# Optimization experiments

Measured on AMD Instinct MI355X. Metric: run time of the kernel, lower is better.

## Reference

```python
import jax, jax.numpy as jnp
import numpy as np

B, S, D, H, L, MLP, WIN = 4, 1024, 256, 8, 2, 1024, 64
HD = D // H
NEG = -1e9  # emulates -inf additive mask; exp underflows to exact 0

_idx = jnp.arange(S)
BAND = jnp.where(jnp.abs(_idx[:, None] - _idx[None, :]) <= WIN, 0.0, NEG).astype(jnp.float32)


def setup_inputs() -> dict:
    key = jax.random.key(0)
    ks = iter(jax.random.split(key, 16))
    r = lambda shape, s=0.02: jax.random.normal(next(ks), shape, dtype=jnp.float32) * s
    return {
        "x": jax.random.normal(next(ks), (B, S, D), dtype=jnp.float32),
        "scale": jnp.ones((1,), jnp.float32) * (D ** -0.5),
        "Win_a": r((L, 3 * D, D)), "bin_a": jnp.zeros((L, 3 * D), jnp.float32),
        "Wout_a": r((L, D, D)), "bout_a": jnp.zeros((L, D), jnp.float32),
        "Win_e": r((L, 3 * D, D)), "bin_e": jnp.zeros((L, 3 * D), jnp.float32),
        "Wout_e": r((L, D, D)), "bout_e": jnp.zeros((L, D), jnp.float32),
        "ln1_g": jnp.ones((L, D), jnp.float32), "ln1_b": jnp.zeros((L, D), jnp.float32),
        "ln2_g": jnp.ones((L, D), jnp.float32), "ln2_b": jnp.zeros((L, D), jnp.float32),
        "W1": r((L, MLP, D)), "b1": jnp.zeros((L, MLP), jnp.float32),
        "W2": r((L, D, MLP)), "b2": jnp.zeros((L, D), jnp.float32),
        "lnf_g": jnp.ones((D,), jnp.float32), "lnf_b": jnp.zeros((D,), jnp.float32),
    }


def _layernorm(x, g, b, eps=1e-5):
    m = jnp.mean(x, axis=-1, keepdims=True)
    v = jnp.mean(jnp.square(x - m), axis=-1, keepdims=True)
    return (x - m) * jax.lax.rsqrt(v + eps) * g + b


def _mha(x, Win, bin_, Wout, bout, mask=None):
    # torch nn.MultiheadAttention (batch_first=True), dropout=0
    b, s, _ = x.shape
    qkv = x @ Win.T + bin_                       # (b, s, 3D)
    q, k, v = jnp.split(qkv, 3, axis=-1)
    split = lambda t: t.reshape(b, s, H, HD).transpose(0, 2, 1, 3)  # (b, H, s, HD)
    q, k, v = split(q), split(k), split(v)
    scores = jnp.einsum('bhqd,bhkd->bhqk', q, k) / np.float32(np.sqrt(HD))
    if mask is not None:
        scores = scores + mask
    attn = jax.nn.softmax(scores, axis=-1)
    out = jnp.einsum('bhqk,bhkd->bhqd', attn, v).transpose(0, 2, 1, 3).reshape(b, s, D)
    return out @ Wout.T + bout


def reference(x, scale, Win_a, bin_a, Wout_a, bout_a, Win_e, bin_e, Wout_e, bout_e,
              ln1_g, ln1_b, ln2_g, ln2_b, W1, b1, W2, b2, lnf_g, lnf_b):
    # ScaledSinusoidalPositionalEncoding returns arange(S)*scale, shape (S,1)
    pos = jnp.arange(S, dtype=jnp.float32) * scale[0]   # (S,)
    x = x + pos[:, None]                                 # broadcast (B,S,D)+(S,1)
    for l in range(L):
        xi = _mha(x, Win_a[l], bin_a[l], Wout_a[l], bout_a[l])
        x = _layernorm(x + xi, ln1_g[l], ln1_b[l])
        xe = _mha(x, Win_e[l], bin_e[l], Wout_e[l], bout_e[l], mask=BAND)
        attended = _layernorm(x + xe, ln2_g[l], ln2_b[l])
        h = jax.nn.gelu(attended @ W1[l].T + b1[l], approximate=False)
        x = attended + h @ W2[l].T + b2[l]
    return _layernorm(x, lnf_g, lnf_b)
```

## Files before the change

kernel.cpp:

```cpp
#include <hip/hip_runtime.h>
#include <math.h>

#define BB 4
#define SS 1024
#define DD 256
#define HH 8
#define HD 32
#define D3 768
#define MLP 1024
#define NTOK (BB * SS)
#define NSEG 4

typedef __attribute__((ext_vector_type(8))) short short8;
typedef __attribute__((ext_vector_type(4))) float f32x4;

__device__ __forceinline__ unsigned short f2bfu(float f) {
    union { float f; unsigned i; } u; u.f = f;
    unsigned r = u.i + 0x7fffu + ((u.i >> 16) & 1u);
    return (unsigned short)(r >> 16);
}
__device__ __forceinline__ float bfu2f(unsigned short h) {
    union { unsigned i; float f; } u; u.i = ((unsigned)h) << 16; return u.f;
}

#define W_TOT 2097152
#define WL0   196608
__global__ __launch_bounds__(256) void conv_weights(
    const float* __restrict__ a0, const float* __restrict__ a1,
    const float* __restrict__ a2, const float* __restrict__ a3,
    const float* __restrict__ a4, const float* __restrict__ a5,
    unsigned short* __restrict__ out, unsigned short* __restrict__ out_lo)
{
    int i = blockIdx.x * 256 + threadIdx.x;
    const float* s; int off;
    if      (i <  393216) { s = a0; off = 0;       }
    else if (i <  524288) { s = a1; off = 393216;  }
    else if (i <  917504) { s = a2; off = 524288;  }
    else if (i < 1048576) { s = a3; off = 917504;  }
    else if (i < 1572864) { s = a4; off = 1048576; }
    else                  { s = a5; off = 1572864; }
    float v = s[i - off];
    unsigned short h = f2bfu(v);
    out[i] = h;
    if (i < WL0) out_lo[i] = f2bfu(v - bfu2f(h));
}

__global__ __launch_bounds__(256) void add_pos_kernel(
    const float* __restrict__ x, const float* __restrict__ scale,
    float* __restrict__ out, unsigned short* __restrict__ outh,
    unsigned short* __restrict__ outl, int n)
{
    int i = blockIdx.x * 256 + threadIdx.x;
    if (i >= n) return;
    int s = (i >> 8) & (SS - 1);
    float v = x[i] + (float)s * scale[0];
    out[i] = v;
    unsigned short h = f2bfu(v);
    outh[i] = h;
    outl[i] = f2bfu(v - bfu2f(h));
}

__device__ __forceinline__ size_t vt_index(int row, int col512) {
    int b = row >> 10, s = row & (SS - 1);
    int h = col512 >> 5, d = col512 & (HD - 1);
    return (((size_t)b * HH + h) * HD + d) * SS + s;
}

#define LDP 40
__global__ __launch_bounds__(256) void gemm_mfma(
    const unsigned short* __restrict__ A, const unsigned short* __restrict__ W,
    const float* __restrict__ bias, const float* __restrict__ resid,
    float* __restrict__ outf, unsigned short* __restrict__ outb,
    unsigned short* __restrict__ vth,
    int M, int N, int K, int act)
{
    __shared__ __align__(16) unsigned short As[64 * LDP];
    __shared__ __align__(16) unsigned short Bs[128 * LDP];
    const int t = threadIdx.x;
    const int lane = t & 63, wave = t >> 6;
    const int wr = wave >> 1, wc = wave & 1;
    const int m0 = blockIdx.y * 64, n0 = blockIdx.x * 128;
    const int sr = t >> 2;
    const int sc = (t & 3) * 8;

    const unsigned short* Ag = A + (size_t)(m0 + sr) * K + sc;
    const unsigned short* Wg = W + (size_t)(n0 + sr) * K + sc;

    f32x4 acc[2][4];
    #pragma unroll
    for (int i = 0; i < 2; i++)
        #pragma unroll
        for (int j = 0; j < 4; j++)
            acc[i][j] = (f32x4){0.f, 0.f, 0.f, 0.f};

    const int lm = lane & 15, lk = (lane >> 4) * 8;

    uint4 a0 = *(const uint4*)(Ag);
    uint4 b0 = *(const uint4*)(Wg);
    uint4 b1 = *(const uint4*)(Wg + (size_t)64 * K);

    for (int k0 = 0; k0 < K; k0 += 32) {
        __syncthreads();
        *(uint4*)&As[sr * LDP + sc]        = a0;
        *(uint4*)&Bs[sr * LDP + sc]        = b0;
        *(uint4*)&Bs[(sr + 64) * LDP + sc] = b1;
        __syncthreads();
        if (k0 + 32 < K) {
            a0 = *(const uint4*)(Ag + k0 + 32);
            b0 = *(const uint4*)(Wg + k0 + 32);
            b1 = *(const uint4*)(Wg + (size_t)64 * K + k0 + 32);
        }

        short8 af[2], bf[4];
        #pragma unroll
        for (int i = 0; i < 2; i++)
            af[i] = *(const short8*)&As[(wr * 32 + i * 16 + lm) * LDP + lk];
        #pragma unroll
        for (int j = 0; j < 4; j++)
            bf[j] = *(const short8*)&Bs[(wc * 64 + j * 16 + lm) * LDP + lk];
        #pragma unroll
        for (int i = 0; i < 2; i++)
            #pragma unroll
            for (int j = 0; j < 4; j++)
                acc[i][j] = __builtin_amdgcn_mfma_f32_16x16x32_bf16(
                    af[i], bf[j], acc[i][j], 0, 0, 0);
    }

    const int lq = lane >> 4;
    #pragma unroll
    for (int j = 0; j < 4; j++) {
        int col = n0 + wc * 64 + j * 16 + lm;
        float bv = bias[col];
        #pragma unroll
        for (int i = 0; i < 2; i++) {
            #pragma unroll
            for (int r = 0; r < 4; r++) {
                int row = m0 + wr * 32 + i * 16 + lq * 4 + r;
                float v = acc[i][j][r] + bv;
                if (act) v = 0.5f * v * (1.0f + erff(v * 0.70710678118654752f));
                if (vth && col >= 2 * DD) {
                    vth[vt_index(row, col - 2 * DD)] = f2bfu(v);
                } else {
                    size_t idx = (size_t)row * N + col;
                    if (resid) v += resid[idx];
                    if (outf) outf[idx] = v;
                    if (outb) outb[idx] = f2bfu(v);
                }
            }
        }
    }
}

__global__ __launch_bounds__(256) void gemm_wout_combine(
    const float* __restrict__ Of, const float2* __restrict__ Ml,
    const unsigned short* __restrict__ W, const float* __restrict__ bias,
    float* __restrict__ outf)
{
    __shared__ __align__(16) unsigned short As[64 * LDP];
    __shared__ __align__(16) unsigned short Bs[128 * LDP];
    const int t = threadIdx.x;
    const int lane = t & 63, wave = t >> 6;
    const int wr = wave >> 1, wc = wave & 1;
    const int m0 = blockIdx.y * 64, n0 = blockIdx.x * 128;
    const int sr = t >> 2;
    const int sc = (t & 3) * 8;
    const int token = m0 + sr;

    const unsigned short* Wg = W + (size_t)(n0 + sr) * DD + sc;

    f32x4 acc[2][4];
    #pragma unroll
    for (int i = 0; i < 2; i++)
        #pragma unroll
        for (int j = 0; j < 4; j++)
            acc[i][j] = (f32x4){0.f, 0.f, 0.f, 0.f};

    const int lm = lane & 15, lk = (lane >> 4) * 8;

    for (int k0 = 0; k0 < DD; k0 += 32) {
        const int h = (k0 + sc) >> 5;
        float2 ml[NSEG];
        float M = -1e30f;
        #pragma unroll
        for (int s = 0; s < NSEG; s++) {
            ml[s] = Ml[((size_t)s * NTOK + token) * HH + h];
            M = fmaxf(M, ml[s].x);
        }
        float wgt[NSEG]; float denom = 0.f;
        #pragma unroll
        for (int s = 0; s < NSEG; s++) {
            wgt[s] = __expf(ml[s].x - M);
            denom += ml[s].y * wgt[s];
        }
        const float inv = 1.0f / denom;
        float a8[8] = {};
        #pragma unroll
        for (int s = 0; s < NSEG; s++) {
            const float* p = Of + ((size_t)s * NTOK + token) * DD + k0 + sc;
            float4 x0 = *(const float4*)p;
            float4 x1 = *(const float4*)(p + 4);
            a8[0] += x0.x * wgt[s]; a8[1] += x0.y * wgt[s];
            a8[2] += x0.z * wgt[s]; a8[3] += x0.w * wgt[s];
            a8[4] += x1.x * wgt[s]; a8[5] += x1.y * wgt[s];
            a8[6] += x1.z * wgt[s]; a8[7] += x1.w * wgt[s];
        }
        unsigned short ab[8];
        #pragma unroll
        for (int c = 0; c < 8; c++) ab[c] = f2bfu(a8[c] * inv);

        uint4 b0 = *(const uint4*)(Wg + k0);
        uint4 b1 = *(const uint4*)(Wg + (size_t)64 * DD + k0);
        __syncthreads();
        #pragma unroll
        for (int c = 0; c < 8; c++) As[sr * LDP + sc + c] = ab[c];
        *(uint4*)&Bs[sr * LDP + sc]        = b0;
        *(uint4*)&Bs[(sr + 64) * LDP + sc] = b1;
        __syncthreads();

        short8 af[2], bf[4];
        #pragma unroll
        for (int i = 0; i < 2; i++)
            af[i] = *(const short8*)&As[(wr * 32 + i * 16 + lm) * LDP + lk];
        #pragma unroll
        for (int j = 0; j < 4; j++)
            bf[j] = *(const short8*)&Bs[(wc * 64 + j * 16 + lm) * LDP + lk];
        #pragma unroll
        for (int i = 0; i < 2; i++)
            #pragma unroll
            for (int j = 0; j < 4; j++)
                acc[i][j] = __builtin_amdgcn_mfma_f32_16x16x32_bf16(
                    af[i], bf[j], acc[i][j], 0, 0, 0);
    }

    const int lq = lane >> 4;
    #pragma unroll
    for (int j = 0; j < 4; j++) {
        int col = n0 + wc * 64 + j * 16 + lm;
        float bv = bias[col];
        #pragma unroll
        for (int i = 0; i < 2; i++) {
            #pragma unroll
            for (int r = 0; r < 4; r++) {
                int row = m0 + wr * 32 + i * 16 + lq * 4 + r;
                outf[(size_t)row * DD + col] = acc[i][j][r] + bv;
            }
        }
    }
}

__global__ __launch_bounds__(256) void gemm_mfma_split(
    const unsigned short* __restrict__ Ah, const unsigned short* __restrict__ Al,
    const unsigned short* __restrict__ Wh, const unsigned short* __restrict__ Wl,
    const float* __restrict__ bias,
    unsigned short* __restrict__ outh, unsigned short* __restrict__ outl,
    unsigned short* __restrict__ vth, unsigned short* __restrict__ vtl,
    int M, int N, int K)
{
    __shared__ __align__(16) unsigned short Ash[64 * LDP];
    __shared__ __align__(16) unsigned short Asl[64 * LDP];
    __shared__ __align__(16) unsigned short Bsh[128 * LDP];
    __shared__ __align__(16) unsigned short Bsl[128 * LDP];
    const int t = threadIdx.x;
    const int lane = t & 63, wave = t >> 6;
    const int wr = wave >> 1, wc = wave & 1;
    const int m0 = blockIdx.y * 64, n0 = blockIdx.x * 128;
    const int sr = t >> 2;
    const int sc = (t & 3) * 8;

    const size_t oA = (size_t)(m0 + sr) * K + sc;
    const size_t oW = (size_t)(n0 + sr) * K + sc;

    f32x4 acc[2][4];
    #pragma unroll
    for (int i = 0; i < 2; i++)
        #pragma unroll
        for (int j = 0; j < 4; j++)
            acc[i][j] = (f32x4){0.f, 0.f, 0.f, 0.f};

    const int lm = lane & 15, lk = (lane >> 4) * 8;

    uint4 ah0 = *(const uint4*)(Ah + oA);
    uint4 al0 = *(const uint4*)(Al + oA);
    uint4 bh0 = *(const uint4*)(Wh + oW);
    uint4 bh1 = *(const uint4*)(Wh + oW + (size_t)64 * K);
    uint4 bl0 = *(const uint4*)(Wl + oW);
    uint4 bl1 = *(const uint4*)(Wl + oW + (size_t)64 * K);

    for (int k0 = 0; k0 < K; k0 += 32) {
        __syncthreads();
        *(uint4*)&Ash[sr * LDP + sc]        = ah0;
        *(uint4*)&Asl[sr * LDP + sc]        = al0;
        *(uint4*)&Bsh[sr * LDP + sc]        = bh0;
        *(uint4*)&Bsh[(sr + 64) * LDP + sc] = bh1;
        *(uint4*)&Bsl[sr * LDP + sc]        = bl0;
        *(uint4*)&Bsl[(sr + 64) * LDP + sc] = bl1;
        __syncthreads();
        if (k0 + 32 < K) {
            ah0 = *(const uint4*)(Ah + oA + k0 + 32);
            al0 = *(const uint4*)(Al + oA + k0 + 32);
            bh0 = *(const uint4*)(Wh + oW + k0 + 32);
            bh1 = *(const uint4*)(Wh + oW + (size_t)64 * K + k0 + 32);
            bl0 = *(const uint4*)(Wl + oW + k0 + 32);
            bl1 = *(const uint4*)(Wl + oW + (size_t)64 * K + k0 + 32);
        }

        short8 afh[2], afl[2], bfh[4], bfl[4];
        #pragma unroll
        for (int i = 0; i < 2; i++) {
            afh[i] = *(const short8*)&Ash[(wr * 32 + i * 16 + lm) * LDP + lk];
            afl[i] = *(const short8*)&Asl[(wr * 32 + i * 16 + lm) * LDP + lk];
        }
        #pragma unroll
        for (int j = 0; j < 4; j++) {
            bfh[j] = *(const short8*)&Bsh[(wc * 64 + j * 16 + lm) * LDP + lk];
            bfl[j] = *(const short8*)&Bsl[(wc * 64 + j * 16 + lm) * LDP + lk];
        }
        #pragma unroll
        for (int i = 0; i < 2; i++)
            #pragma unroll
            for (int j = 0; j < 4; j++) {
                acc[i][j] = __builtin_amdgcn_mfma_f32_16x16x32_bf16(
                    afl[i], bfh[j], acc[i][j], 0, 0, 0);
                acc[i][j] = __builtin_amdgcn_mfma_f32_16x16x32_bf16(
                    afh[i], bfl[j], acc[i][j], 0, 0, 0);
                acc[i][j] = __builtin_amdgcn_mfma_f32_16x16x32_bf16(
                    afh[i], bfh[j], acc[i][j], 0, 0, 0);
            }
    }

    const int lq = lane >> 4;
    #pragma unroll
    for (int j = 0; j < 4; j++) {
        int col = n0 + wc * 64 + j * 16 + lm;
        float bv = bias[col];
        #pragma unroll
        for (int i = 0; i < 2; i++) {
            #pragma unroll
            for (int r = 0; r < 4; r++) {
                int row = m0 + wr * 32 + i * 16 + lq * 4 + r;
                float v = acc[i][j][r] + bv;
                unsigned short h = f2bfu(v);
                unsigned short lo = f2bfu(v - bfu2f(h));
                if (col >= 2 * DD) {
                    size_t vi = vt_index(row, col - 2 * DD);
                    vth[vi] = h; vtl[vi] = lo;
                } else {
                    size_t idx = (size_t)row * N + col;
                    outh[idx] = h; outl[idx] = lo;
                }
            }
        }
    }
}

__global__ __launch_bounds__(256) void attn_split(
    const unsigned short* __restrict__ qkvh,
    const unsigned short* __restrict__ qkvl,
    const unsigned short* __restrict__ vth,
    const unsigned short* __restrict__ vtl,
    float* __restrict__ Of, float2* __restrict__ Ml)
{
    __shared__ __align__(16) unsigned short Ks [64 * 40];
    __shared__ __align__(16) unsigned short Vt [32 * 72];
    __shared__ __align__(16) unsigned short Ps [64 * 72];
    __shared__ __align__(16) unsigned short Ksl[64 * 40];
    __shared__ __align__(16) unsigned short Vtl[32 * 72];

    const int t = threadIdx.x;
    const int wave = t >> 6, lane = t & 63;
    const int lm = lane & 15, quad = lane >> 4;
    const int i0 = blockIdx.x * 64, h = blockIdx.y;
    const int z = blockIdx.z;
    const int b = z >> 2, seg = z & (NSEG - 1);
    const int sr = t >> 2, sc8 = (t & 3) * 8;
    const int vd = t >> 3, vs8 = (t & 7) * 8;

    const size_t qoff = ((size_t)(b * SS) + i0 + 16 * wave + lm) * D3 + h * HD + quad * 8;
    short8 qh = *(const short8*)(qkvh + qoff);
    short8 ql = *(const short8*)(qkvl + qoff);

    const unsigned short* Kg  = qkvh + (size_t)(b * SS) * D3 + DD + h * HD;
    const unsigned short* Klg = qkvl + (size_t)(b * SS) * D3 + DD + h * HD;
    const unsigned short* Vg  = vth + ((size_t)b * HH + h) * HD * SS;
    const unsigned short* Vlg = vtl + ((size_t)b * HH + h) * HD * SS;

    float m[4], l[4];
    f32x4 o[2];
    #pragma unroll
    for (int r = 0; r < 4; r++) { m[r] = -1e30f; l[r] = 0.f; }
    o[0] = (f32x4){0.f, 0.f, 0.f, 0.f};
    o[1] = (f32x4){0.f, 0.f, 0.f, 0.f};

    const int per = (SS / 64) / NSEG;
    const int s0 = seg * per, s1 = s0 + per - 1;
    const float scl = 0.17677669529663688f;

    short8 kreg  = *(const short8*)(Kg  + (size_t)(s0 * 64 + sr) * D3 + sc8);
    short8 kregl = *(const short8*)(Klg + (size_t)(s0 * 64 + sr) * D3 + sc8);
    short8 vreg  = *(const short8*)(Vg  + (size_t)vd * SS + s0 * 64 + vs8);
    short8 vregl = *(const short8*)(Vlg + (size_t)vd * SS + s0 * 64 + vs8);

    for (int kt = s0; kt <= s1; kt++) {
        const int k0 = kt * 64;
        __syncthreads();
        *(short8*)&Ks [sr * 40 + sc8] = kreg;
        *(short8*)&Ksl[sr * 40 + sc8] = kregl;
        *(short8*)&Vt [vd * 72 + vs8] = vreg;
        *(short8*)&Vtl[vd * 72 + vs8] = vregl;
        __syncthreads();
        if (kt < s1) {
            kreg  = *(const short8*)(Kg  + (size_t)(k0 + 64 + sr) * D3 + sc8);
            kregl = *(const short8*)(Klg + (size_t)(k0 + 64 + sr) * D3 + sc8);
            vreg  = *(const short8*)(Vg  + (size_t)vd * SS + k0 + 64 + vs8);
            vregl = *(const short8*)(Vlg + (size_t)vd * SS + k0 + 64 + vs8);
        }

        f32x4 s[4];
        #pragma unroll
        for (int cb = 0; cb < 4; cb++) {
            short8 kf  = *(const short8*)&Ks [(16 * cb + lm) * 40 + quad * 8];
            short8 kfl = *(const short8*)&Ksl[(16 * cb + lm) * 40 + quad * 8];
            f32x4 a = (f32x4){0.f, 0.f, 0.f, 0.f};
            a = __builtin_amdgcn_mfma_f32_16x16x32_bf16(ql, kf,  a, 0, 0, 0);
            a = __builtin_amdgcn_mfma_f32_16x16x32_bf16(qh, kfl, a, 0, 0, 0);
            a = __builtin_amdgcn_mfma_f32_16x16x32_bf16(qh, kf,  a, 0, 0, 0);
            s[cb] = a;
        }

        #pragma unroll
        for (int r = 0; r < 4; r++) {
            float s0r = s[0][r] * scl, s1r = s[1][r] * scl;
            float s2r = s[2][r] * scl, s3r = s[3][r] * scl;
            float tm = fmaxf(fmaxf(s0r, s1r), fmaxf(s2r, s3r));
            tm = fmaxf(tm, __shfl_xor(tm, 1, 64));
            tm = fmaxf(tm, __shfl_xor(tm, 2, 64));
            tm = fmaxf(tm, __shfl_xor(tm, 4, 64));
            tm = fmaxf(tm, __shfl_xor(tm, 8, 64));
            float mn = fmaxf(m[r], tm);
            float alpha = __expf(m[r] - mn);
            float p0 = __expf(s0r - mn), p1 = __expf(s1r - mn);
            float p2 = __expf(s2r - mn), p3 = __expf(s3r - mn);
            float ps = p0 + p1 + p2 + p3;
            ps += __shfl_xor(ps, 1, 64);
            ps += __shfl_xor(ps, 2, 64);
            ps += __shfl_xor(ps, 4, 64);
            ps += __shfl_xor(ps, 8, 64);
            l[r] = l[r] * alpha + ps;
            o[0][r] *= alpha;
            o[1][r] *= alpha;
            m[r] = mn;
            const int pr = (16 * wave + quad * 4 + r) * 72 + lm;
            Ps[pr +  0] = f2bfu(p0);
            Ps[pr + 16] = f2bfu(p1);
            Ps[pr + 32] = f2bfu(p2);
            Ps[pr + 48] = f2bfu(p3);
        }

        #pragma unroll
        for (int kc = 0; kc < 2; kc++) {
            short8 pf = *(const short8*)&Ps[(16 * wave + lm) * 72 + 32 * kc + quad * 8];
            #pragma unroll
            for (int nh = 0; nh < 2; nh++) {
                short8 vf  = *(const short8*)&Vt [(16 * nh + lm) * 72 + 32 * kc + quad * 8];
                short8 vfl = *(const short8*)&Vtl[(16 * nh + lm) * 72 + 32 * kc + quad * 8];
                o[nh] = __builtin_amdgcn_mfma_f32_16x16x32_bf16(pf, vf,  o[nh], 0, 0, 0);
                o[nh] = __builtin_amdgcn_mfma_f32_16x16x32_bf16(pf, vfl, o[nh], 0, 0, 0);
            }
        }
    }

    #pragma unroll
    for (int r = 0; r < 4; r++) {
        int row = i0 + 16 * wave + quad * 4 + r;
        size_t base = ((size_t)seg * NTOK + b * SS + row) * DD + h * HD + lm;
        Of[base]      = o[0][r];
        Of[base + 16] = o[1][r];
        if (lm == 0)
            Ml[((size_t)seg * NTOK + b * SS + row) * HH + h] =
                make_float2(m[r], l[r]);
    }
}

__global__ __launch_bounds__(256) void attn_fixed(
    const unsigned short* __restrict__ qkvh,
    const unsigned short* __restrict__ vth,
    unsigned short* __restrict__ outb,
    float* __restrict__ Of, float2* __restrict__ Ml,
    int win, int nseg)
{
    __shared__ __align__(16) unsigned short Ks[64 * 40];
    __shared__ __align__(16) unsigned short Vt[32 * 72];
    __shared__ __align__(16) unsigned short Ps[64 * 72];

    const int t = threadIdx.x;
    const int wave = t >> 6, lane = t & 63;
    const int lm = lane & 15, quad = lane >> 4;
    const int i0 = blockIdx.x * 64, h = blockIdx.y;
    const int z = blockIdx.z;
    const int b = z / nseg, seg = z - b * nseg;
    const int sr = t >> 2, sc8 = (t & 3) * 8;
    const int vd = t >> 3, vs8 = (t & 7) * 8;

    const size_t qoff = ((size_t)(b * SS) + i0 + 16 * wave + lm) * D3 + h * HD + quad * 8;
    short8 qh = *(const short8*)(qkvh + qoff);

    const unsigned short* Kg = qkvh + (size_t)(b * SS) * D3 + DD + h * HD;
    const unsigned short* Vg = vth + ((size_t)b * HH + h) * HD * SS;

    float l[4] = {0.f, 0.f, 0.f, 0.f};
    f32x4 o[2];
    o[0] = (f32x4){0.f, 0.f, 0.f, 0.f};
    o[1] = (f32x4){0.f, 0.f, 0.f, 0.f};

    int t0 = 0, t1 = SS / 64 - 1;
    const bool masked = (win < SS);
    if (masked) {
        t0 = (i0 - win) >> 6;        if (t0 < 0) t0 = 0;
        t1 = (i0 + 63 + win) >> 6;   if (t1 > SS / 64 - 1) t1 = SS / 64 - 1;
    }
    const int per = (t1 - t0 + nseg) / nseg;
    const int s0 = t0 + seg * per;
    const int s1 = (s0 + per - 1 < t1) ? (s0 + per - 1) : t1;
    const float scl = 0.17677669529663688f;
    const float M0 = 32.0f;

    short8 kreg = *(const short8*)(Kg + (size_t)(s0 * 64 + sr) * D3 + sc8);
    short8 vreg = *(const short8*)(Vg + (size_t)vd * SS + s0 * 64 + vs8);

    for (int kt = s0; kt <= s1; kt++) {
        const int k0 = kt * 64;
        __syncthreads();
        *(short8*)&Ks[sr * 40 + sc8] = kreg;
        *(short8*)&Vt[vd * 72 + vs8] = vreg;
        __syncthreads();
        if (kt < s1) {
            kreg = *(const short8*)(Kg + (size_t)(k0 + 64 + sr) * D3 + sc8);
            vreg = *(const short8*)(Vg + (size_t)vd * SS + k0 + 64 + vs8);
        }

        f32x4 s[4];
        #pragma unroll
        for (int cb = 0; cb < 4; cb++) {
            short8 kf = *(const short8*)&Ks[(16 * cb + lm) * 40 + quad * 8];
            f32x4 a = (f32x4){0.f, 0.f, 0.f, 0.f};
            a = __builtin_amdgcn_mfma_f32_16x16x32_bf16(qh, kf, a, 0, 0, 0);
            s[cb] = a;
        }

        #pragma unroll
        for (int r = 0; r < 4; r++) {
            float p[4];
            #pragma unroll
            for (int cb = 0; cb < 4; cb++) {
                float v = s[cb][r] * scl;
                if (masked) {
                    int di = (i0 + 16 * wave + quad * 4 + r) - (k0 + 16 * cb + lm);
                    if (di > win || di < -win) v = -1e30f;
                }
                p[cb] = __expf(v - M0);
            }
            l[r] += p[0] + p[1] + p[2] + p[3];
            const int pr = (16 * wave + quad * 4 + r) * 72 + lm;
            Ps[pr +  0] = f2bfu(p[0]);
            Ps[pr + 16] = f2bfu(p[1]);
            Ps[pr + 32] = f2bfu(p[2]);
            Ps[pr + 48] = f2bfu(p[3]);
        }

        #pragma unroll
        for (int kc = 0; kc < 2; kc++) {
            short8 pf = *(const short8*)&Ps[(16 * wave + lm) * 72 + 32 * kc + quad * 8];
            #pragma unroll
            for (int nh = 0; nh < 2; nh++) {
                short8 vf = *(const short8*)&Vt[(16 * nh + lm) * 72 + 32 * kc + quad * 8];
                o[nh] = __builtin_amdgcn_mfma_f32_16x16x32_bf16(pf, vf, o[nh], 0, 0, 0);
            }
        }
    }

    #pragma unroll
    for (int r = 0; r < 4; r++) {
        l[r] += __shfl_xor(l[r], 1, 64);
        l[r] += __shfl_xor(l[r], 2, 64);
        l[r] += __shfl_xor(l[r], 4, 64);
        l[r] += __shfl_xor(l[r], 8, 64);
    }

    if (nseg == 1) {
        #pragma unroll
        for (int r = 0; r < 4; r++) {
            float invl = 1.0f / l[r];
            size_t base = ((size_t)(b * SS) + i0 + 16 * wave + quad * 4 + r) * DD + h * HD + lm;
            outb[base]      = f2bfu(o[0][r] * invl);
            outb[base + 16] = f2bfu(o[1][r] * invl);
        }
    } else {
        #pragma unroll
        for (int r = 0; r < 4; r++) {
            int row = i0 + 16 * wave + quad * 4 + r;
            size_t base = ((size_t)seg * NTOK + b * SS + row) * DD + h * HD + lm;
            Of[base]      = o[0][r];
            Of[base + 16] = o[1][r];
            if (lm == 0)
                Ml[((size_t)seg * NTOK + b * SS + row) * HH + h] =
                    make_float2(M0, l[r]);
        }
    }
}

__global__ __launch_bounds__(256) void ln_kernel(
    const float* __restrict__ a, const float* __restrict__ r,
    const float* __restrict__ g, const float* __restrict__ bt,
    float* __restrict__ outf, unsigned short* __restrict__ outb)
{
    const int wave = threadIdx.x >> 6, lane = threadIdx.x & 63;
    const int row = blockIdx.x * 4 + wave;
    const size_t base = (size_t)row * DD + lane * 4;
    float4 v = *(const float4*)(a + base);
    if (r) {
        float4 rv = *(const float4*)(r + base);
        v.x += rv.x; v.y += rv.y; v.z += rv.z; v.w += rv.w;
    }
    float s = v.x + v.y + v.z + v.w;
    #pragma unroll
    for (int off = 1; off < 64; off <<= 1) s += __shfl_xor(s, off, 64);
    float mean = s * (1.0f / 256.0f);
    float4 dv = { v.x - mean, v.y - mean, v.z - mean, v.w - mean };
    float s2 = dv.x * dv.x + dv.y * dv.y + dv.z * dv.z + dv.w * dv.w;
    #pragma unroll
    for (int off = 1; off < 64; off <<= 1) s2 += __shfl_xor(s2, off, 64);
    float rst = rsqrtf(s2 * (1.0f / 256.0f) + 1e-5f);
    float4 g4 = *(const float4*)(g + lane * 4);
    float4 b4 = *(const float4*)(bt + lane * 4);
    float4 ov = { dv.x * rst * g4.x + b4.x, dv.y * rst * g4.y + b4.y,
                  dv.z * rst * g4.z + b4.z, dv.w * rst * g4.w + b4.w };
    if (outf) *(float4*)(outf + base) = ov;
    if (outb) {
        ushort4 u = { f2bfu(ov.x), f2bfu(ov.y), f2bfu(ov.z), f2bfu(ov.w) };
        *(ushort4*)(outb + base) = u;
    }
}

extern "C" void kernel_launch(void* const* d_in, const int* in_sizes, int n_in,
                              void* d_out, int out_size, void* d_ws, size_t ws_size,
                              hipStream_t stream)
{
    const float* xin   = (const float*)d_in[0];
    const float* scale = (const float*)d_in[1];
    const float* Win_a = (const float*)d_in[2];
    const float* bin_a = (const float*)d_in[3];
    const float* Wout_a= (const float*)d_in[4];
    const float* bout_a= (const float*)d_in[5];
    const float* Win_e = (const float*)d_in[6];
    const float* bin_e = (const float*)d_in[7];
    const float* Wout_e= (const float*)d_in[8];
    const float* bout_e= (const float*)d_in[9];
    const float* ln1_g = (const float*)d_in[10];
    const float* ln1_b = (const float*)d_in[11];
    const float* ln2_g = (const float*)d_in[12];
    const float* ln2_b = (const float*)d_in[13];
    const float* W1    = (const float*)d_in[14];
    const float* b1    = (const float*)d_in[15];
    const float* W2    = (const float*)d_in[16];
    const float* b2    = (const float*)d_in[17];
    const float* lnf_g = (const float*)d_in[18];
    const float* lnf_b = (const float*)d_in[19];

    char* ws = (char*)d_ws;
    float* X    = (float*)ws;                     ws += (size_t)NTOK * DD * 4;
    float* X2   = (float*)ws;                     ws += (size_t)NTOK * DD * 4;
    float* P    = (float*)ws;                     ws += (size_t)NTOK * DD * 4;
    unsigned short* Xb   = (unsigned short*)ws;   ws += (size_t)NTOK * DD * 2;
    unsigned short* Xlb  = (unsigned short*)ws;   ws += (size_t)NTOK * DD * 2;
    unsigned short* X2b  = (unsigned short*)ws;   ws += (size_t)NTOK * DD * 2;
    unsigned short* ATb  = (unsigned short*)ws;   ws += (size_t)NTOK * DD * 2;
    unsigned short* QKVb = (unsigned short*)ws;   ws += (size_t)NTOK * D3 * 2;
    unsigned short* QKVl = (unsigned short*)ws;   ws += (size_t)NTOK * D3 * 2;
    unsigned short* VTh  = (unsigned short*)ws;   ws += (size_t)NTOK * DD * 2;
    unsigned short* VTl  = (unsigned short*)ws;   ws += (size_t)NTOK * DD * 2;
    unsigned short* HMLb = (unsigned short*)ws;   ws += (size_t)NTOK * MLP * 2;
    unsigned short* Wb   = (unsigned short*)ws;   ws += (size_t)W_TOT * 2;
    unsigned short* Wl0  = (unsigned short*)ws;   ws += (size_t)WL0 * 2;
    float2* Ml           = (float2*)ws;           ws += (size_t)NSEG * NTOK * HH * 8;
    float* Of            = (float*)ws;            ws += (size_t)NSEG * NTOK * DD * 4;

    unsigned short* WinA_b  = Wb + 0;
    unsigned short* WoutA_b = Wb + 393216;
    unsigned short* WinE_b  = Wb + 524288;
    unsigned short* WoutE_b = Wb + 917504;
    unsigned short* W1_b    = Wb + 1048576;
    unsigned short* W2_b    = Wb + 1572864;

    conv_weights<<<W_TOT / 256, 256, 0, stream>>>(
        Win_a, Wout_a, Win_e, Wout_e, W1, W2, Wb, Wl0);
    add_pos_kernel<<<(NTOK * DD + 255) / 256, 256, 0, stream>>>(
        xin, scale, X, Xb, Xlb, NTOK * DD);

    float* cur = X;            float* oth = X2;
    unsigned short* curb = Xb; unsigned short* othb = X2b;

    for (int l = 0; l < 2; l++) {
        if (l == 0) {
            gemm_mfma_split<<<dim3(D3 / 128, NTOK / 64), 256, 0, stream>>>(
                Xb, Xlb, WinA_b, Wl0, bin_a, QKVb, QKVl, VTh, VTl, NTOK, D3, DD);
            attn_split<<<dim3(SS / 64, HH, BB * NSEG), 256, 0, stream>>>(
                QKVb, QKVl, VTh, VTl, Of, Ml);
        } else {
            gemm_mfma<<<dim3(D3 / 128, NTOK / 64), 256, 0, stream>>>(
                curb, WinA_b + (size_t)l * D3 * DD, bin_a + (size_t)l * D3,
                nullptr, nullptr, QKVb, VTh, NTOK, D3, DD, 0);
            attn_fixed<<<dim3(SS / 64, HH, BB * NSEG), 256, 0, stream>>>(
                QKVb, VTh, nullptr, Of, Ml, 1 << 28, NSEG);
        }
        gemm_wout_combine<<<dim3(DD / 128, NTOK / 64), 256, 0, stream>>>(
            Of, Ml, WoutA_b + (size_t)l * DD * DD, bout_a + (size_t)l * DD, P);
        ln_kernel<<<NTOK / 4, 256, 0, stream>>>(
            P, cur, ln1_g + l * DD, ln1_b + l * DD, oth, othb);

        gemm_mfma<<<dim3(D3 / 128, NTOK / 64), 256, 0, stream>>>(
            othb, WinE_b + (size_t)l * D3 * DD, bin_e + (size_t)l * D3,
            nullptr, nullptr, QKVb, VTh, NTOK, D3, DD, 0);
        attn_fixed<<<dim3(SS / 64, HH, BB), 256, 0, stream>>>(
            QKVb, VTh, ATb, nullptr, nullptr, 64, 1);
        gemm_mfma<<<dim3(DD / 128, NTOK / 64), 256, 0, stream>>>(
            ATb, WoutE_b + (size_t)l * DD * DD, bout_e + (size_t)l * DD,
            nullptr, P, nullptr, nullptr, NTOK, DD, DD, 0);
        ln_kernel<<<NTOK / 4, 256, 0, stream>>>(
            P, oth, ln2_g + l * DD, ln2_b + l * DD, cur, curb);

        gemm_mfma<<<dim3(MLP / 128, NTOK / 64), 256, 0, stream>>>(
            curb, W1_b + (size_t)l * MLP * DD, b1 + (size_t)l * MLP,
            nullptr, nullptr, HMLb, nullptr, NTOK, MLP, DD, 1);
        gemm_mfma<<<dim3(DD / 128, NTOK / 64), 256, 0, stream>>>(
            HMLb, W2_b + (size_t)l * DD * MLP, b2 + (size_t)l * DD,
            cur, oth, othb, nullptr, NTOK, DD, MLP, 0);

        float* tf = cur; cur = oth; oth = tf;
        unsigned short* tb = curb; curb = othb; othb = tb;
    }

    ln_kernel<<<NTOK / 4, 256, 0, stream>>>(cur, nullptr, lnf_g, lnf_b,
                                            (float*)d_out, nullptr);
}
```

Before: 351.5 us.

## Fuse LayerNorm into full-row output GEMMs and drop low-precision V split

Adds a templated gemm_ln kernel in which each block computes a full 256-wide output row tile, so it can add bias and residual and apply LayerNorm in the epilogue. This replaces the separate Wout GEMM (or Wout-combine) plus ln_kernel pairs, and also fuses the final W2 GEMM with the final LayerNorm. The fp32 intermediate P round trip and several launches go away. It also removes the bf16 low-part correction for V in the layer-0 split-precision attention, halving its V loads and PV MFMAs at some accuracy cost. The trade-off is that the fused GEMMs launch only 64 blocks, each with more accumulators, which reduces parallelism.

```diff
diff --git a/kernel.cpp b/kernel.cpp
--- a/kernel.cpp
+++ b/kernel.cpp
@@ -151,100 +151,171 @@
     }
 }
 
-__global__ __launch_bounds__(256) void gemm_wout_combine(
+template<bool COMBINE>
+__global__ __launch_bounds__(256) void gemm_ln(
+    const unsigned short* __restrict__ A,
     const float* __restrict__ Of, const float2* __restrict__ Ml,
     const unsigned short* __restrict__ W, const float* __restrict__ bias,
-    float* __restrict__ outf)
+    const float* __restrict__ resid,
+    const float* __restrict__ g, const float* __restrict__ bt,
+    float* __restrict__ outf, unsigned short* __restrict__ outb, int K)
 {
     __shared__ __align__(16) unsigned short As[64 * LDP];
-    __shared__ __align__(16) unsigned short Bs[128 * LDP];
+    __shared__ __align__(16) unsigned short Bs[256 * LDP];
+    __shared__ float rsum[2][64];
+    __shared__ float rsum2[2][64];
     const int t = threadIdx.x;
     const int lane = t & 63, wave = t >> 6;
     const int wr = wave >> 1, wc = wave & 1;
-    const int m0 = blockIdx.y * 64, n0 = blockIdx.x * 128;
+    const int m0 = blockIdx.x * 64;
     const int sr = t >> 2;
     const int sc = (t & 3) * 8;
     const int token = m0 + sr;
 
-    const unsigned short* Wg = W + (size_t)(n0 + sr) * DD + sc;
-
-    f32x4 acc[2][4];
+    const unsigned short* Ag = COMBINE ? nullptr : A + (size_t)(m0 + sr) * K + sc;
+    const unsigned short* Wg = W + (size_t)sr * K + sc;
+
+    f32x4 acc[2][8];
     #pragma unroll
     for (int i = 0; i < 2; i++)
         #pragma unroll
-        for (int j = 0; j < 4; j++)
+        for (int j = 0; j < 8; j++)
             acc[i][j] = (f32x4){0.f, 0.f, 0.f, 0.f};
 
     const int lm = lane & 15, lk = (lane >> 4) * 8;
 
-    for (int k0 = 0; k0 < DD; k0 += 32) {
-        const int h = (k0 + sc) >> 5;
-        float2 ml[NSEG];
-        float M = -1e30f;
-        #pragma unroll
-        for (int s = 0; s < NSEG; s++) {
-            ml[s] = Ml[((size_t)s * NTOK + token) * HH + h];
-            M = fmaxf(M, ml[s].x);
-        }
-        float wgt[NSEG]; float denom = 0.f;
-        #pragma unroll
-        for (int s = 0; s < NSEG; s++) {
-            wgt[s] = __expf(ml[s].x - M);
-            denom += ml[s].y * wgt[s];
-        }
-        const float inv = 1.0f / denom;
-        float a8[8] = {};
-        #pragma unroll
-        for (int s = 0; s < NSEG; s++) {
-            const float* p = Of + ((size_t)s * NTOK + token) * DD + k0 + sc;
-            float4 x0 = *(const float4*)p;
-            float4 x1 = *(const float4*)(p + 4);
-            a8[0] += x0.x * wgt[s]; a8[1] += x0.y * wgt[s];
-            a8[2] += x0.z * wgt[s]; a8[3] += x0.w * wgt[s];
-            a8[4] += x1.x * wgt[s]; a8[5] += x1.y * wgt[s];
-            a8[6] += x1.z * wgt[s]; a8[7] += x1.w * wgt[s];
-        }
+    for (int k0 = 0; k0 < K; k0 += 32) {
         unsigned short ab[8];
-        #pragma unroll
-        for (int c = 0; c < 8; c++) ab[c] = f2bfu(a8[c] * inv);
-
+        if (COMBINE) {
+            const int h = (k0 + sc) >> 5;
+            float2 ml[NSEG];
+            float M = -1e30f;
+            #pragma unroll
+            for (int s = 0; s < NSEG; s++) {
+                ml[s] = Ml[((size_t)s * NTOK + token) * HH + h];
+                M = fmaxf(M, ml[s].x);
+            }
+            float wgt[NSEG]; float denom = 0.f;
+            #pragma unroll
+            for (int s = 0; s < NSEG; s++) {
+                wgt[s] = __expf(ml[s].x - M);
+                denom += ml[s].y * wgt[s];
+            }
+            const float inv = 1.0f / denom;
+            float a8[8] = {};
+            #pragma unroll
+            for (int s = 0; s < NSEG; s++) {
+                const float* p = Of + ((size_t)s * NTOK + token) * DD + k0 + sc;
+                float4 x0 = *(const float4*)p;
+                float4 x1 = *(const float4*)(p + 4);
+                a8[0] += x0.x * wgt[s]; a8[1] += x0.y * wgt[s];
+                a8[2] += x0.z * wgt[s]; a8[3] += x0.w * wgt[s];
+                a8[4] += x1.x * wgt[s]; a8[5] += x1.y * wgt[s];
+                a8[6] += x1.z * wgt[s]; a8[7] += x1.w * wgt[s];
+            }
+            #pragma unroll
+            for (int c = 0; c < 8; c++) ab[c] = f2bfu(a8[c] * inv);
+        } else {
+            uint4 av = *(const uint4*)(Ag + k0);
+            *(uint4*)ab = av;
+        }
         uint4 b0 = *(const uint4*)(Wg + k0);
-        uint4 b1 = *(const uint4*)(Wg + (size_t)64 * DD + k0);
-        __syncthreads();
-        #pragma unroll
-        for (int c = 0; c < 8; c++) As[sr * LDP + sc + c] = ab[c];
-        *(uint4*)&Bs[sr * LDP + sc]        = b0;
-        *(uint4*)&Bs[(sr + 64) * LDP + sc] = b1;
-        __syncthreads();
-
-        short8 af[2], bf[4];
+        uint4 b1 = *(const uint4*)(Wg + (size_t)64 * K + k0);
+        uint4 b2 = *(const uint4*)(Wg + (size_t)128 * K + k0);
+        uint4 b3 = *(const uint4*)(Wg + (size_t)192 * K + k0);
+        __syncthreads();
+        *(uint4*)&As[sr * LDP + sc] = *(uint4*)ab;
+        *(uint4*)&Bs[sr * LDP + sc]         = b0;
+        *(uint4*)&Bs[(sr + 64) * LDP + sc]  = b1;
+        *(uint4*)&Bs[(sr + 128) * LDP + sc] = b2;
+        *(uint4*)&Bs[(sr + 192) * LDP + sc] = b3;
+        __syncthreads();
+
+        short8 af[2], bf[8];
         #pragma unroll
         for (int i = 0; i < 2; i++)
             af[i] = *(const short8*)&As[(wr * 32 + i * 16 + lm) * LDP + lk];
         #pragma unroll
-        for (int j = 0; j < 4; j++)
-            bf[j] = *(const short8*)&Bs[(wc * 64 + j * 16 + lm) * LDP + lk];
+        for (int j = 0; j < 8; j++)
+            bf[j] = *(const short8*)&Bs[(wc * 128 + j * 16 + lm) * LDP + lk];
         #pragma unroll
         for (int i = 0; i < 2; i++)
             #pragma unroll
-            for (int j = 0; j < 4; j++)
+            for (int j = 0; j < 8; j++)
                 acc[i][j] = __builtin_amdgcn_mfma_f32_16x16x32_bf16(
                     af[i], bf[j], acc[i][j], 0, 0, 0);
     }
 
     const int lq = lane >> 4;
     #pragma unroll
-    for (int j = 0; j < 4; j++) {
-        int col = n0 + wc * 64 + j * 16 + lm;
+    for (int j = 0; j < 8; j++) {
+        int col = wc * 128 + j * 16 + lm;
         float bv = bias[col];
         #pragma unroll
-        for (int i = 0; i < 2; i++) {
+        for (int i = 0; i < 2; i++)
             #pragma unroll
             for (int r = 0; r < 4; r++) {
                 int row = m0 + wr * 32 + i * 16 + lq * 4 + r;
-                outf[(size_t)row * DD + col] = acc[i][j][r] + bv;
-            }
-        }
+                acc[i][j][r] += bv + resid[(size_t)row * DD + col];
+            }
+    }
+    #pragma unroll
+    for (int i = 0; i < 2; i++)
+        #pragma unroll
+        for (int r = 0; r < 4; r++) {
+            float s = 0.f;
+            #pragma unroll
+            for (int j = 0; j < 8; j++) s += acc[i][j][r];
+            s += __shfl_xor(s, 1, 64); s += __shfl_xor(s, 2, 64);
+            s += __shfl_xor(s, 4, 64); s += __shfl_xor(s, 8, 64);
+            if (lm == 0) rsum[wc][wr * 32 + i * 16 + lq * 4 + r] = s;
+        }
+    __syncthreads();
+    float mean_[2][4];
+    #pragma unroll
+    for (int i = 0; i < 2; i++)
+        #pragma unroll
+        for (int r = 0; r < 4; r++) {
+            int ri = wr * 32 + i * 16 + lq * 4 + r;
+            mean_[i][r] = (rsum[0][ri] + rsum[1][ri]) * (1.0f / 256.0f);
+        }
+    #pragma unroll
+    for (int i = 0; i < 2; i++)
+        #pragma unroll
+        for (int r = 0; r < 4; r++) {
+            float s2 = 0.f;
+            #pragma unroll
+            for (int j = 0; j < 8; j++) {
+                float d = acc[i][j][r] - mean_[i][r];
+                s2 += d * d;
+            }
+            s2 += __shfl_xor(s2, 1, 64); s2 += __shfl_xor(s2, 2, 64);
+            s2 += __shfl_xor(s2, 4, 64); s2 += __shfl_xor(s2, 8, 64);
+            if (lm == 0) rsum2[wc][wr * 32 + i * 16 + lq * 4 + r] = s2;
+        }
+    __syncthreads();
+    float rstd[2][4];
+    #pragma unroll
+    for (int i = 0; i < 2; i++)
+        #pragma unroll
+        for (int r = 0; r < 4; r++) {
+            int ri = wr * 32 + i * 16 + lq * 4 + r;
+            rstd[i][r] = rsqrtf((rsum2[0][ri] + rsum2[1][ri]) * (1.0f / 256.0f) + 1e-5f);
+        }
+    #pragma unroll
+    for (int j = 0; j < 8; j++) {
+        int col = wc * 128 + j * 16 + lm;
+        float gv = g[col], bv2 = bt[col];
+        #pragma unroll
+        for (int i = 0; i < 2; i++)
+            #pragma unroll
+            for (int r = 0; r < 4; r++) {
+                int row = m0 + wr * 32 + i * 16 + lq * 4 + r;
+                float ov = (acc[i][j][r] - mean_[i][r]) * rstd[i][r] * gv + bv2;
+                size_t idx = (size_t)row * DD + col;
+                if (outf) outf[idx] = ov;
+                if (outb) outb[idx] = f2bfu(ov);
+            }
     }
 }
 
@@ -253,7 +324,7 @@
     const unsigned short* __restrict__ Wh, const unsigned short* __restrict__ Wl,
     const float* __restrict__ bias,
     unsigned short* __restrict__ outh, unsigned short* __restrict__ outl,
-    unsigned short* __restrict__ vth, unsigned short* __restrict__ vtl,
+    unsigned short* __restrict__ vth,
     int M, int N, int K)
 {
     __shared__ __align__(16) unsigned short Ash[64 * LDP];
@@ -340,13 +411,12 @@
                 int row = m0 + wr * 32 + i * 16 + lq * 4 + r;
                 float v = acc[i][j][r] + bv;
                 unsigned short h = f2bfu(v);
-                unsigned short lo = f2bfu(v - bfu2f(h));
                 if (col >= 2 * DD) {
-                    size_t vi = vt_index(row, col - 2 * DD);
-                    vth[vi] = h; vtl[vi] = lo;
+                    vth[vt_index(row, col - 2 * DD)] = h;
                 } else {
                     size_t idx = (size_t)row * N + col;
-                    outh[idx] = h; outl[idx] = lo;
+                    outh[idx] = h;
+                    outl[idx] = f2bfu(v - bfu2f(h));
                 }
             }
         }
@@ -357,14 +427,12 @@
     const unsigned short* __restrict__ qkvh,
     const unsigned short* __restrict__ qkvl,
     const unsigned short* __restrict__ vth,
-    const unsigned short* __restrict__ vtl,
     float* __restrict__ Of, float2* __restrict__ Ml)
 {
     __shared__ __align__(16) unsigned short Ks [64 * 40];
     __shared__ __align__(16) unsigned short Vt [32 * 72];
     __shared__ __align__(16) unsigned short Ps [64 * 72];
     __shared__ __align__(16) unsigned short Ksl[64 * 40];
-    __shared__ __align__(16) unsigned short Vtl[32 * 72];
 
     const int t = threadIdx.x;
     const int wave = t >> 6, lane = t & 63;
@@ -382,7 +450,6 @@
     const unsigned short* Kg  = qkvh + (size_t)(b * SS) * D3 + DD + h * HD;
     const unsigned short* Klg = qkvl + (size_t)(b * SS) * D3 + DD + h * HD;
     const unsigned short* Vg  = vth + ((size_t)b * HH + h) * HD * SS;
-    const unsigned short* Vlg = vtl + ((size_t)b * HH + h) * HD * SS;
 
     float m[4], l[4];
     f32x4 o[2];
@@ -398,7 +465,6 @@
     short8 kreg  = *(const short8*)(Kg  + (size_t)(s0 * 64 + sr) * D3 + sc8);
     short8 kregl = *(const short8*)(Klg + (size_t)(s0 * 64 + sr) * D3 + sc8);
     short8 vreg  = *(const short8*)(Vg  + (size_t)vd * SS + s0 * 64 + vs8);
-    short8 vregl = *(const short8*)(Vlg + (size_t)vd * SS + s0 * 64 + vs8);
 
     for (int kt = s0; kt <= s1; kt++) {
         const int k0 = kt * 64;
@@ -406,13 +472,11 @@
         *(short8*)&Ks [sr * 40 + sc8] = kreg;
         *(short8*)&Ksl[sr * 40 + sc8] = kregl;
         *(short8*)&Vt [vd * 72 + vs8] = vreg;
-        *(short8*)&Vtl[vd * 72 + vs8] = vregl;
         __syncthreads();
         if (kt < s1) {
             kreg  = *(const short8*)(Kg  + (size_t)(k0 + 64 + sr) * D3 + sc8);
             kregl = *(const short8*)(Klg + (size_t)(k0 + 64 + sr) * D3 + sc8);
             vreg  = *(const short8*)(Vg  + (size_t)vd * SS + k0 + 64 + vs8);
-            vregl = *(const short8*)(Vlg + (size_t)vd * SS + k0 + 64 + vs8);
         }
 
         f32x4 s[4];
@@ -461,10 +525,8 @@
             short8 pf = *(const short8*)&Ps[(16 * wave + lm) * 72 + 32 * kc + quad * 8];
             #pragma unroll
             for (int nh = 0; nh < 2; nh++) {
-                short8 vf  = *(const short8*)&Vt [(16 * nh + lm) * 72 + 32 * kc + quad * 8];
-                short8 vfl = *(const short8*)&Vtl[(16 * nh + lm) * 72 + 32 * kc + quad * 8];
-                o[nh] = __builtin_amdgcn_mfma_f32_16x16x32_bf16(pf, vf,  o[nh], 0, 0, 0);
-                o[nh] = __builtin_amdgcn_mfma_f32_16x16x32_bf16(pf, vfl, o[nh], 0, 0, 0);
+                short8 vf = *(const short8*)&Vt[(16 * nh + lm) * 72 + 32 * kc + quad * 8];
+                o[nh] = __builtin_amdgcn_mfma_f32_16x16x32_bf16(pf, vf, o[nh], 0, 0, 0);
             }
         }
     }
@@ -605,39 +667,6 @@
                 Ml[((size_t)seg * NTOK + b * SS + row) * HH + h] =
                     make_float2(M0, l[r]);
         }
-    }
-}
-
-__global__ __launch_bounds__(256) void ln_kernel(
-    const float* __restrict__ a, const float* __restrict__ r,
-    const float* __restrict__ g, const float* __restrict__ bt,
-    float* __restrict__ outf, unsigned short* __restrict__ outb)
-{
-    const int wave = threadIdx.x >> 6, lane = threadIdx.x & 63;
-    const int row = blockIdx.x * 4 + wave;
-    const size_t base = (size_t)row * DD + lane * 4;
-    float4 v = *(const float4*)(a + base);
-    if (r) {
-        float4 rv = *(const float4*)(r + base);
-        v.x += rv.x; v.y += rv.y; v.z += rv.z; v.w += rv.w;
-    }
-    float s = v.x + v.y + v.z + v.w;
-    #pragma unroll
-    for (int off = 1; off < 64; off <<= 1) s += __shfl_xor(s, off, 64);
-    float mean = s * (1.0f / 256.0f);
-    float4 dv = { v.x - mean, v.y - mean, v.z - mean, v.w - mean };
-    float s2 = dv.x * dv.x + dv.y * dv.y + dv.z * dv.z + dv.w * dv.w;
-    #pragma unroll
-    for (int off = 1; off < 64; off <<= 1) s2 += __shfl_xor(s2, off, 64);
-    float rst = rsqrtf(s2 * (1.0f / 256.0f) + 1e-5f);
-    float4 g4 = *(const float4*)(g + lane * 4);
-    float4 b4 = *(const float4*)(bt + lane * 4);
-    float4 ov = { dv.x * rst * g4.x + b4.x, dv.y * rst * g4.y + b4.y,
-                  dv.z * rst * g4.z + b4.z, dv.w * rst * g4.w + b4.w };
-    if (outf) *(float4*)(outf + base) = ov;
-    if (outb) {
-        ushort4 u = { f2bfu(ov.x), f2bfu(ov.y), f2bfu(ov.z), f2bfu(ov.w) };
-        *(ushort4*)(outb + base) = u;
     }
 }
 
@@ -669,7 +698,6 @@
     char* ws = (char*)d_ws;
     float* X    = (float*)ws;                     ws += (size_t)NTOK * DD * 4;
     float* X2   = (float*)ws;                     ws += (size_t)NTOK * DD * 4;
-    float* P    = (float*)ws;                     ws += (size_t)NTOK * DD * 4;
     unsigned short* Xb   = (unsigned short*)ws;   ws += (size_t)NTOK * DD * 2;
     unsigned short* Xlb  = (unsigned short*)ws;   ws += (size_t)NTOK * DD * 2;
     unsigned short* X2b  = (unsigned short*)ws;   ws += (size_t)NTOK * DD * 2;
@@ -677,7 +705,6 @@
     unsigned short* QKVb = (unsigned short*)ws;   ws += (size_t)NTOK * D3 * 2;
     unsigned short* QKVl = (unsigned short*)ws;   ws += (size_t)NTOK * D3 * 2;
     unsigned short* VTh  = (unsigned short*)ws;   ws += (size_t)NTOK * DD * 2;
-    unsigned short* VTl  = (unsigned short*)ws;   ws += (size_t)NTOK * DD * 2;
     unsigned short* HMLb = (unsigned short*)ws;   ws += (size_t)NTOK * MLP * 2;
     unsigned short* Wb   = (unsigned short*)ws;   ws += (size_t)W_TOT * 2;
     unsigned short* Wl0  = (unsigned short*)ws;   ws += (size_t)WL0 * 2;
@@ -702,9 +729,9 @@
     for (int l = 0; l < 2; l++) {
         if (l == 0) {
             gemm_mfma_split<<<dim3(D3 / 128, NTOK / 64), 256, 0, stream>>>(
-                Xb, Xlb, WinA_b, Wl0, bin_a, QKVb, QKVl, VTh, VTl, NTOK, D3, DD);
+                Xb, Xlb, WinA_b, Wl0, bin_a, QKVb, QKVl, VTh, NTOK, D3, DD);
             attn_split<<<dim3(SS / 64, HH, BB * NSEG), 256, 0, stream>>>(
-                QKVb, QKVl, VTh, VTl, Of, Ml);
+                QKVb, QKVl, VTh, Of, Ml);
         } else {
             gemm_mfma<<<dim3(D3 / 128, NTOK / 64), 256, 0, stream>>>(
                 curb, WinA_b + (size_t)l * D3 * DD, bin_a + (size_t)l * D3,
@@ -712,33 +739,35 @@
             attn_fixed<<<dim3(SS / 64, HH, BB * NSEG), 256, 0, stream>>>(
                 QKVb, VTh, nullptr, Of, Ml, 1 << 28, NSEG);
         }
-        gemm_wout_combine<<<dim3(DD / 128, NTOK / 64), 256, 0, stream>>>(
-            Of, Ml, WoutA_b + (size_t)l * DD * DD, bout_a + (size_t)l * DD, P);
-        ln_kernel<<<NTOK / 4, 256, 0, stream>>>(
-            P, cur, ln1_g + l * DD, ln1_b + l * DD, oth, othb);
+        gemm_ln<true><<<NTOK / 64, 256, 0, stream>>>(
+            nullptr, Of, Ml, WoutA_b + (size_t)l * DD * DD,
+            bout_a + (size_t)l * DD, cur,
+            ln1_g + l * DD, ln1_b + l * DD, oth, othb, DD);
 
         gemm_mfma<<<dim3(D3 / 128, NTOK / 64), 256, 0, stream>>>(
             othb, WinE_b + (size_t)l * D3 * DD, bin_e + (size_t)l * D3,
             nullptr, nullptr, QKVb, VTh, NTOK, D3, DD, 0);
         attn_fixed<<<dim3(SS / 64, HH, BB), 256, 0, stream>>>(
             QKVb, VTh, ATb, nullptr, nullptr, 64, 1);
-        gemm_mfma<<<dim3(DD / 128, NTOK / 64), 256, 0, stream>>>(
-            ATb, WoutE_b + (size_t)l * DD * DD, bout_e + (size_t)l * DD,
-            nullptr, P, nullptr, nullptr, NTOK, DD, DD, 0);
-        ln_kernel<<<NTOK / 4, 256, 0, stream>>>(
-            P, oth, ln2_g + l * DD, ln2_b + l * DD, cur, curb);
+        gemm_ln<false><<<NTOK / 64, 256, 0, stream>>>(
+            ATb, nullptr, nullptr, WoutE_b + (size_t)l * DD * DD,
+            bout_e + (size_t)l * DD, oth,
+            ln2_g + l * DD, ln2_b + l * DD, cur, curb, DD);
 
         gemm_mfma<<<dim3(MLP / 128, NTOK / 64), 256, 0, stream>>>(
             curb, W1_b + (size_t)l * MLP * DD, b1 + (size_t)l * MLP,
             nullptr, nullptr, HMLb, nullptr, NTOK, MLP, DD, 1);
-        gemm_mfma<<<dim3(DD / 128, NTOK / 64), 256, 0, stream>>>(
-            HMLb, W2_b + (size_t)l * DD * MLP, b2 + (size_t)l * DD,
-            cur, oth, othb, nullptr, NTOK, DD, MLP, 0);
-
-        float* tf = cur; cur = oth; oth = tf;
-        unsigned short* tb = curb; curb = othb; othb = tb;
-    }
-
-    ln_kernel<<<NTOK / 4, 256, 0, stream>>>(cur, nullptr, lnf_g, lnf_b,
-                                            (float*)d_out, nullptr);
-}
+        if (l == 0) {
+            gemm_mfma<<<dim3(DD / 128, NTOK / 64), 256, 0, stream>>>(
+                HMLb, W2_b + (size_t)l * DD * MLP, b2 + (size_t)l * DD,
+                cur, oth, othb, nullptr, NTOK, DD, MLP, 0);
+            float* tf = cur; cur = oth; oth = tf;
+            unsigned short* tb = curb; curb = othb; othb = tb;
+        } else {
+            gemm_ln<false><<<NTOK / 64, 256, 0, stream>>>(
+                HMLb, nullptr, nullptr, W2_b + (size_t)l * DD * MLP,
+                b2 + (size_t)l * DD, cur,
+                lnf_g, lnf_b, (float*)d_out, nullptr, MLP);
+        }
+    }
+}
```

Result: slower. 373.2 us (+6.2%).
